# Kernel optimization log

Measured on AMD Instinct MI355X. Metric: run time of the kernel, lower is better.

## Reference

```python
import jax, jax.numpy as jnp
import numpy as np
import math

B, S, P, G = 8, 512, 64, 64
E, GE = 768, 32          # sub_embed_dim, gene_embed_dim
HD = E // 2              # sub_head_dim = 384
L = P * G
LAMBDA_INIT = 0.8 - 0.6 * math.exp(-0.3 * 0)  # depth=0 -> 0.2
SCALING = HD ** -0.5


def setup_inputs() -> dict:
    key0 = jax.random.key(0)
    ks = jax.random.split(key0, 12)
    init = 0.02
    return {
        "query": jax.random.normal(ks[0], (B, S, E), jnp.float32),
        "key": jax.random.normal(ks[1], (B, P, G, GE), jnp.float32),
        "query_mask": jax.random.bernoulli(ks[2], 0.9, (B, S)),
        "key_mask": jax.random.bernoulli(ks[3], 0.9, (B, P, G)),
        # weights stored [in, out] so y = x @ W (equiv to torch Linear no-bias)
        "Wq": jax.random.normal(ks[4], (E, E), jnp.float32) * init,
        "Wkv": jax.random.normal(ks[5], (GE, 2 * E), jnp.float32) * init,
        "Wout": jax.random.normal(ks[6], (E, E), jnp.float32) * init,
        "lambda_q1": jax.random.normal(ks[7], (HD,), jnp.float32) * 0.1,
        "lambda_k1": jax.random.normal(ks[8], (HD,), jnp.float32) * 0.1,
        "lambda_q2": jax.random.normal(ks[9], (HD,), jnp.float32) * 0.1,
        "lambda_k2": jax.random.normal(ks[10], (HD,), jnp.float32) * 0.1,
        "ln_weight": jnp.ones((E,), jnp.float32),  # RMSNorm affine weight (2*HD = E)
    }


def reference(query, key, query_mask, key_mask, Wq, Wkv, Wout,
              lambda_q1, lambda_k1, lambda_q2, lambda_k2, ln_weight):
    # Projections
    Q = query @ Wq                                   # [B,S,E]
    KV = key.reshape(B, L, GE) @ Wkv                 # [B,L,2E]
    K = KV[..., :E]                                  # [B,L,E]
    V = KV[..., E:]                                  # [B,L,E] (= 2*HD)

    # Split into 2 heads of dim HD
    Qh = Q.reshape(B, S, 2, HD).transpose(0, 2, 1, 3) * SCALING   # [B,2,S,HD]
    Kh = K.reshape(B, L, 2, HD).transpose(0, 2, 1, 3)             # [B,2,L,HD]

    # Combined mask [B,S,L]
    mask = query_mask[:, :, None] & key_mask.reshape(B, L)[:, None, :]

    # Dual attention scores + stable softmax (eps=1e-8 on denominator)
    scores = jnp.einsum('bhsd,bhld->bhsl', Qh, Kh)                # [B,2,S,L]
    scores = jnp.where(mask[:, None], scores, -1e20)
    m = jnp.max(scores, axis=-1, keepdims=True)
    p = jnp.exp(scores - m)
    attn = p / (jnp.sum(p, axis=-1, keepdims=True) + 1e-8)

    # Differential combination
    lam = (jnp.exp(jnp.sum(lambda_q1 * lambda_k1))
           - jnp.exp(jnp.sum(lambda_q2 * lambda_k2)) + LAMBDA_INIT)
    diff = attn[:, 0] - lam * attn[:, 1]                          # [B,S,L]
    diff = diff - jnp.min(diff, axis=-1, keepdims=True) + 1e-20
    diff = jnp.where(mask, diff, 0.0)

    # Value contraction: [B,S,L] @ [B,L,E] -> [B,S,E]
    attn_out = jnp.einsum('bsl,ble->bse', diff, V)

    # RMSNorm (eps=1e-5, affine) then scale by (1 - lambda_init)
    ms = jnp.mean(attn_out * attn_out, axis=-1, keepdims=True)
    attn_out = attn_out * jax.lax.rsqrt(ms + 1e-5) * ln_weight
    attn_out = attn_out * (1.0 - LAMBDA_INIT)

    out = attn_out @ Wout                                         # [B,S,E]
    return out, diff.reshape(B, S, P, G)
```

## Files before the change

### kernel.cpp

```cpp
#include <hip/hip_runtime.h>
#include <math.h>

#define LAM_INIT 0.2f
#define ONE_MINUS_LAM 0.8f
#define SCALING_F 0.05103103630798288f

typedef _Float16 h2 __attribute__((ext_vector_type(2)));

#if defined(__has_builtin)
#if __has_builtin(__builtin_amdgcn_fdot2)
#define FDOT2(a, b, c) __builtin_amdgcn_fdot2((a), (b), (c), false)
#endif
#endif
#ifndef FDOT2
#define FDOT2(a, b, c) ((float)(a).x * (float)(b).x + ((float)(a).y * (float)(b).y + (c)))
#endif

__device__ inline float waveMin(float v) {
#pragma unroll
    for (int o = 32; o > 0; o >>= 1) v = fminf(v, __shfl_xor(v, o));
    return v;
}
__device__ inline float waveSum(float v) {
#pragma unroll
    for (int o = 32; o > 0; o >>= 1) v += __shfl_xor(v, o);
    return v;
}

__global__ __launch_bounds__(256) void k01_prep(
    const float* __restrict__ key, const float* __restrict__ Wq,
    const float* __restrict__ Wkv, const float* __restrict__ Wout,
    const float* __restrict__ lq1, const float* __restrict__ lk1,
    const float* __restrict__ lq2, const float* __restrict__ lk2,
    const float* __restrict__ ln,
    unsigned* __restrict__ keyThU, float* __restrict__ Wcp,
    float* __restrict__ Wvp, float* __restrict__ lam)
{
    int blk = blockIdx.x;
    int tid = threadIdx.x;
    if (blk < 128) {
        int b  = blk >> 4;
        int l0 = (blk & 15) << 8;
        __shared__ float tile[256 * 33];
        const float* kp = key + ((size_t)b * 4096 + l0) * 32;
#pragma unroll
        for (int q = 0; q < 32; ++q) {
            int idx = tid + (q << 8);
            int r = idx >> 5, g = idx & 31;
            tile[r * 33 + g] = kp[idx];
        }
        __syncthreads();
#pragma unroll
        for (int gp = 0; gp < 16; ++gp) {
            h2 v;
            v.x = (_Float16)tile[tid * 33 + 2 * gp];
            v.y = (_Float16)tile[tid * 33 + 2 * gp + 1];
            keyThU[((size_t)(b * 16 + gp)) * 4096 + l0 + tid] =
                __builtin_bit_cast(unsigned, v);
        }
    } else if (blk < 512) {
        int bb = blk - 128;
        int kc = bb & 1;
        int ob = bb >> 1;
        int idx = ob * 256 + tid;
        int e  = idx >> 6;
        int hg = idx & 63;
        int h = hg >> 5, g = hg & 31;
        const float4* wqr = (const float4*)(Wq  + (size_t)e * 768 + h * 384 + kc * 192);
        const float4* wkr = (const float4*)(Wkv + (size_t)g * 1536 + h * 384 + kc * 192);
        float s0 = 0.f, s1 = 0.f;
#pragma unroll 4
        for (int d = 0; d < 48; d += 2) {
            float4 a0 = wqr[d],   b0 = wkr[d];
            float4 a1 = wqr[d+1], b1 = wkr[d+1];
            s0 += a0.x*b0.x + a0.y*b0.y + a0.z*b0.z + a0.w*b0.w;
            s1 += a1.x*b1.x + a1.y*b1.y + a1.z*b1.z + a1.w*b1.w;
        }
        Wcp[kc * 49152 + idx] = (s0 + s1) * SCALING_F;
    } else if (blk < 1280) {
        int bb = blk - 512;
        int kc = bb / 96;
        int ob = bb - kc * 96;
        int idx = ob * 256 + tid;
        int g = idx / 768;
        int e = idx - g * 768;
        const float* wvr = Wkv + (size_t)g * 1536 + 768;
        int c0 = kc * 96;
        float s0 = 0.f, s1 = 0.f;
#pragma unroll 4
        for (int c = c0; c < c0 + 96; c += 2) {
            s0 += wvr[c]   * ln[c]   * Wout[(size_t)c * 768 + e];
            s1 += wvr[c+1] * ln[c+1] * Wout[(size_t)(c+1) * 768 + e];
        }
        Wvp[kc * 24576 + idx] = s0 + s1;
    } else {
        float s1 = 0.f, s2 = 0.f;
        for (int d = tid; d < 384; d += 256) {
            s1 += lq1[d] * lk1[d];
            s2 += lq2[d] * lk2[d];
        }
        s1 = waveSum(s1);
        s2 = waveSum(s2);
        __shared__ float r1[4], r2[4];
        int wid = tid >> 6, lane = tid & 63;
        if (lane == 0) { r1[wid] = s1; r2[wid] = s2; }
        __syncthreads();
        if (tid == 0) {
            float a  = r1[0] + r1[1] + r1[2] + r1[3];
            float b2 = r2[0] + r2[1] + r2[2] + r2[3];
            lam[0] = expf(a) - expf(b2) + LAM_INIT;
        }
    }
}

__global__ __launch_bounds__(256) void k2_qt(
    const float* __restrict__ query, const float* __restrict__ Wcp,
    const float* __restrict__ Wvp, float* __restrict__ Wvo,
    float* __restrict__ Qtp)
{
    int blk = blockIdx.x;
    int tid = threadIdx.x;
    if (blk >= 512) {
        int idx = (blk - 512) * 256 + tid;
        float s = 0.f;
#pragma unroll
        for (int kc = 0; kc < 8; ++kc) s += Wvp[kc * 24576 + idx];
        Wvo[idx] = s;
        return;
    }
    int kc = blk >> 7;
    int mt = blk & 127;
    int m0 = mt * 32;
    __shared__ __align__(16) float As[64 * 33];
    __shared__ __align__(16) float Bs[64 * 64];

    int tm = tid >> 5;
    int tn = tid & 31;
    float acc[4][2];
#pragma unroll
    for (int r = 0; r < 4; ++r) { acc[r][0] = 0.f; acc[r][1] = 0.f; }

    for (int ch = 0; ch < 3; ++ch) {
        int k0 = kc * 192 + ch * 64;
        __syncthreads();
#pragma unroll
        for (int q = 0; q < 2; ++q) {
            int f = tid + q * 256;
            int m = f >> 4, kq = f & 15;
            float4 v = *(const float4*)&query[(size_t)(m0 + m) * 768 + k0 + kq * 4];
            As[(kq * 4 + 0) * 33 + m] = v.x;
            As[(kq * 4 + 1) * 33 + m] = v.y;
            As[(kq * 4 + 2) * 33 + m] = v.z;
            As[(kq * 4 + 3) * 33 + m] = v.w;
        }
#pragma unroll
        for (int q = 0; q < 4; ++q) {
            int f = tid + q * 256;
            int kk = f >> 4, n4 = f & 15;
            float4 a = *(const float4*)&Wcp[(size_t)(k0 + kk) * 64 + n4 * 4];
            float4 b = *(const float4*)&Wcp[49152 + (size_t)(k0 + kk) * 64 + n4 * 4];
            float4 s; s.x = a.x + b.x; s.y = a.y + b.y; s.z = a.z + b.z; s.w = a.w + b.w;
            *(float4*)&Bs[kk * 64 + n4 * 4] = s;
        }
        __syncthreads();
#pragma unroll 8
        for (int kk = 0; kk < 64; ++kk) {
            float4 a = *(const float4*)&As[kk * 33 + tm * 4];
            float2 b = *(const float2*)&Bs[kk * 64 + tn * 2];
            acc[0][0] += a.x * b.x; acc[0][1] += a.x * b.y;
            acc[1][0] += a.y * b.x; acc[1][1] += a.y * b.y;
            acc[2][0] += a.z * b.x; acc[2][1] += a.z * b.y;
            acc[3][0] += a.w * b.x; acc[3][1] += a.w * b.y;
        }
    }
#pragma unroll
    for (int r = 0; r < 4; ++r) {
        float2 o; o.x = acc[r][0]; o.y = acc[r][1];
        *(float2*)&Qtp[(size_t)kc * 262144 + (size_t)(m0 + tm * 4 + r) * 64 + tn * 2] = o;
    }
}

__global__ __launch_bounds__(512, 4) void k3_attn(
    const float* __restrict__ Qtp, const unsigned* __restrict__ keyThU,
    const int* __restrict__ qmask, const int* __restrict__ kmask,
    const float* __restrict__ lamp, float* __restrict__ diffO)
{
    int blk = blockIdx.x;
    int b  = blk >> 7;
    int s0 = (blk & 127) * 4;
    int tid = threadIdx.x;
    int lane = tid & 63, wid = tid >> 6;

    __shared__ __align__(16) unsigned qt_th[128];
    __shared__ float redS[64];
    __shared__ float redM[32];

    if (tid < 128) {
        int ts = tid >> 5;
        int h  = (tid >> 4) & 1;
        int gp = tid & 15;
        size_t row = (size_t)(b * 512 + s0 + ts) * 64;
        int col = h * 32 + 2 * gp;
        float v0 = 0.f, v1 = 0.f;
#pragma unroll
        for (int kc = 0; kc < 4; ++kc) {
            v0 += Qtp[(size_t)kc * 262144 + row + col];
            v1 += Qtp[(size_t)kc * 262144 + row + col + 1];
        }
        h2 hv; hv.x = (_Float16)v0; hv.y = (_Float16)v1;
        qt_th[gp * 8 + ts * 2 + h] = __builtin_bit_cast(unsigned, hv);
    }
    int qm[4];
#pragma unroll
    for (int ts = 0; ts < 4; ++ts) qm[ts] = qmask[b * 512 + s0 + ts];
    float lam = lamp[0];

    unsigned kmb = 0;
#pragma unroll
    for (int c = 0; c < 2; ++c) {
        int4 km = *(const int4*)(kmask + b * 4096 + c * 2048 + tid * 4);
        if (km.x) kmb |= 1u << (c * 4 + 0);
        if (km.y) kmb |= 1u << (c * 4 + 1);
        if (km.z) kmb |= 1u << (c * 4 + 2);
        if (km.w) kmb |= 1u << (c * 4 + 3);
    }
    __syncthreads();

    float p[2][4][8];
#pragma unroll
    for (int h = 0; h < 2; ++h)
#pragma unroll
        for (int ts = 0; ts < 4; ++ts)
#pragma unroll
            for (int i = 0; i < 8; ++i) p[h][ts][i] = 0.f;

    const unsigned* kt = keyThU + (size_t)b * 16 * 4096 + tid * 4;
    for (int gp = 0; gp < 16; ++gp) {
        uint4 q0 = *(const uint4*)&qt_th[gp * 8];
        uint4 q1 = *(const uint4*)&qt_th[gp * 8 + 4];
        h2 qv[8];
        qv[0] = __builtin_bit_cast(h2, q0.x); qv[1] = __builtin_bit_cast(h2, q0.y);
        qv[2] = __builtin_bit_cast(h2, q0.z); qv[3] = __builtin_bit_cast(h2, q0.w);
        qv[4] = __builtin_bit_cast(h2, q1.x); qv[5] = __builtin_bit_cast(h2, q1.y);
        qv[6] = __builtin_bit_cast(h2, q1.z); qv[7] = __builtin_bit_cast(h2, q1.w);
        const unsigned* kg = kt + (size_t)gp * 4096;
#pragma unroll
        for (int c = 0; c < 2; ++c) {
            uint4 kv = *(const uint4*)(kg + c * 2048);
            h2 k0 = __builtin_bit_cast(h2, kv.x);
            h2 k1 = __builtin_bit_cast(h2, kv.y);
            h2 k2 = __builtin_bit_cast(h2, kv.z);
            h2 k3 = __builtin_bit_cast(h2, kv.w);
#pragma unroll
            for (int ts = 0; ts < 4; ++ts)
#pragma unroll
                for (int h = 0; h < 2; ++h) {
                    h2 q = qv[ts * 2 + h];
                    p[h][ts][c*4+0] = FDOT2(k0, q, p[h][ts][c*4+0]);
                    p[h][ts][c*4+1] = FDOT2(k1, q, p[h][ts][c*4+1]);
                    p[h][ts][c*4+2] = FDOT2(k2, q, p[h][ts][c*4+2]);
                    p[h][ts][c*4+3] = FDOT2(k3, q, p[h][ts][c*4+3]);
                }
        }
    }

    float inv[2][4];
#pragma unroll
    for (int h = 0; h < 2; ++h)
#pragma unroll
        for (int ts = 0; ts < 4; ++ts) {
            float s = 0.f;
#pragma unroll
            for (int i = 0; i < 8; ++i) {
                bool ok = qm[ts] && ((kmb >> i) & 1u);
                float e = ok ? __expf(p[h][ts][i]) : 0.f;
                p[h][ts][i] = e;
                s += e;
            }
            s = waveSum(s);
            if (lane == 0) redS[(h * 4 + ts) * 8 + wid] = s;
        }
    __syncthreads();
#pragma unroll
    for (int h = 0; h < 2; ++h)
#pragma unroll
        for (int ts = 0; ts < 4; ++ts) {
            int r = (h * 4 + ts) * 8;
            float s = redS[r];
#pragma unroll
            for (int w = 1; w < 8; ++w) s += redS[r + w];
            inv[h][ts] = 1.0f / (s + 1e-8f);
        }

    float mn[4];
#pragma unroll
    for (int ts = 0; ts < 4; ++ts) {
        float v = 3.4e38f;
#pragma unroll
        for (int i = 0; i < 8; ++i) {
            float d = p[0][ts][i] * inv[0][ts] - lam * (p[1][ts][i] * inv[1][ts]);
            p[0][ts][i] = d;
            v = fminf(v, d);
        }
        v = waveMin(v);
        if (lane == 0) redM[ts * 8 + wid] = v;
    }
    __syncthreads();
#pragma unroll
    for (int ts = 0; ts < 4; ++ts) {
        int r = ts * 8;
        float v = redM[r];
#pragma unroll
        for (int w = 1; w < 8; ++w) v = fminf(v, redM[r + w]);
        mn[ts] = v;
    }

#pragma unroll
    for (int ts = 0; ts < 4; ++ts) {
        size_t base = (size_t)(b * 512 + s0 + ts) * 4096 + tid * 4;
#pragma unroll
        for (int c = 0; c < 2; ++c) {
            float4 o;
            float v0 = p[0][ts][c*4+0] - mn[ts] + 1e-20f;
            float v1 = p[0][ts][c*4+1] - mn[ts] + 1e-20f;
            float v2 = p[0][ts][c*4+2] - mn[ts] + 1e-20f;
            float v3 = p[0][ts][c*4+3] - mn[ts] + 1e-20f;
            o.x = (qm[ts] && ((kmb >> (c*4+0)) & 1u)) ? v0 : 0.f;
            o.y = (qm[ts] && ((kmb >> (c*4+1)) & 1u)) ? v1 : 0.f;
            o.z = (qm[ts] && ((kmb >> (c*4+2)) & 1u)) ? v2 : 0.f;
            o.w = (qm[ts] && ((kmb >> (c*4+3)) & 1u)) ? v3 : 0.f;
            *(float4*)(diffO + base + c * 2048) = o;
        }
    }
}

__global__ __launch_bounds__(256) void k4_T(
    const float* __restrict__ diff, const float* __restrict__ key,
    float* __restrict__ P)
{
    int blk = blockIdx.x;
    int rt = blk & 63, kc = blk >> 6;
    int row0 = rt << 6;
    int b = row0 >> 9;
    int l0 = kc << 9;
    int tid = threadIdx.x;
    int tx = tid & 7;
    int ty = tid >> 3;
    int g0 = tx * 4;

    __shared__ __align__(16) float Ks[256][32];

    float acc[2][4];
#pragma unroll
    for (int r = 0; r < 2; ++r)
#pragma unroll
        for (int c2 = 0; c2 < 4; ++c2) acc[r][c2] = 0.f;

    for (int ph = 0; ph < 2; ++ph) {
        int lp = l0 + ph * 256;
        __syncthreads();
#pragma unroll
        for (int q = 0; q < 32; ++q) {
            int idx = tid + (q << 8);
            int r = idx >> 5, g = idx & 31;
            Ks[r][g] = key[((size_t)(b * 4096 + lp + r)) * 32 + g];
        }
        __syncthreads();

        for (int j4 = 0; j4 < 64; ++j4) {
            int l = lp + j4 * 4;
            float4 dv[2];
#pragma unroll
            for (int r = 0; r < 2; ++r)
                dv[r] = *(const float4*)(diff + (size_t)(row0 + ty * 2 + r) * 4096 + l);
#pragma unroll
            for (int jj = 0; jj < 4; ++jj) {
                float4 kq = *(const float4*)&Ks[j4 * 4 + jj][g0];
#pragma unroll
                for (int r = 0; r < 2; ++r) {
                    float d = (jj == 0) ? dv[r].x : (jj == 1) ? dv[r].y : (jj == 2) ? dv[r].z : dv[r].w;
                    acc[r][0] += d * kq.x;
                    acc[r][1] += d * kq.y;
                    acc[r][2] += d * kq.z;
                    acc[r][3] += d * kq.w;
                }
            }
        }
    }
#pragma unroll
    for (int r = 0; r < 2; ++r) {
        float4 o; o.x = acc[r][0]; o.y = acc[r][1]; o.z = acc[r][2]; o.w = acc[r][3];
        *(float4*)&P[(size_t)kc * 131072 + (size_t)(row0 + ty * 2 + r) * 32 + g0] = o;
    }
}

__global__ __launch_bounds__(256, 4) void k5_out(
    const float* __restrict__ P, const float* __restrict__ Wkv,
    const float* __restrict__ Wvo, float* __restrict__ out)
{
    int row0 = blockIdx.x * 4;
    int tid = threadIdx.x;
    int w = tid >> 6;
    int lane = tid & 63;
    __shared__ __align__(16) float Ts[4][32];

    if (tid < 128) {
        int r = tid >> 5, g = tid & 31;
        float s = 0.f;
#pragma unroll
        for (int kc = 0; kc < 8; ++kc)
            s += P[(size_t)kc * 131072 + (size_t)(row0 + r) * 32 + g];
        Ts[r][g] = s;
    }
    __syncthreads();

    float4 t[8];
#pragma unroll
    for (int q = 0; q < 8; ++q) t[q] = *(const float4*)&Ts[w][q * 4];

    float ssq = 0.f;
#pragma unroll 2
    for (int j = 0; j < 12; ++j) {
        int e = lane + j * 64;
        const float* wp = Wkv + 768 + e;
        float a = 0.f;
#pragma unroll
        for (int q = 0; q < 8; ++q) {
            a += t[q].x * wp[(size_t)(q * 4 + 0) * 1536];
            a += t[q].y * wp[(size_t)(q * 4 + 1) * 1536];
            a += t[q].z * wp[(size_t)(q * 4 + 2) * 1536];
            a += t[q].w * wp[(size_t)(q * 4 + 3) * 1536];
        }
        ssq += a * a;
    }
    ssq = waveSum(ssq);
    float rs = rsqrtf(ssq * (1.0f / 768.0f) + 1e-5f) * ONE_MINUS_LAM;

#pragma unroll 2
    for (int j = 0; j < 12; ++j) {
        int e = lane + j * 64;
        const float* wp = Wvo + e;
        float o = 0.f;
#pragma unroll
        for (int q = 0; q < 8; ++q) {
            o += t[q].x * wp[(size_t)(q * 4 + 0) * 768];
            o += t[q].y * wp[(size_t)(q * 4 + 1) * 768];
            o += t[q].z * wp[(size_t)(q * 4 + 2) * 768];
            o += t[q].w * wp[(size_t)(q * 4 + 3) * 768];
        }
        out[(size_t)(row0 + w) * 768 + e] = o * rs;
    }
}

extern "C" void kernel_launch(void* const* d_in, const int* in_sizes, int n_in,
                              void* d_out, int out_size, void* d_ws, size_t ws_size,
                              hipStream_t stream) {
    (void)in_sizes; (void)n_in; (void)out_size; (void)ws_size;
    const float* query = (const float*)d_in[0];
    const float* key   = (const float*)d_in[1];
    const int*   qmask = (const int*)d_in[2];
    const int*   kmask = (const int*)d_in[3];
    const float* Wq    = (const float*)d_in[4];
    const float* Wkv   = (const float*)d_in[5];
    const float* Wout  = (const float*)d_in[6];
    const float* lq1   = (const float*)d_in[7];
    const float* lk1   = (const float*)d_in[8];
    const float* lq2   = (const float*)d_in[9];
    const float* lk2   = (const float*)d_in[10];
    const float* ln    = (const float*)d_in[11];

    float* out  = (float*)d_out;
    float* diff = out + 3145728;

    float* ws      = (float*)d_ws;
    float* Wcp     = ws;
    float* Wvo     = ws + 98304;
    float* Wvp     = ws + 122880;
    float* lam     = ws + 319488;
    unsigned* keyThU = (unsigned*)(ws + 319552);
    float* Qtp     = ws + 843840;
    float* P       = Qtp;

    k01_prep<<<1281, 256, 0, stream>>>(key, Wq, Wkv, Wout, lq1, lk1, lq2, lk2, ln,
                                       keyThU, Wcp, Wvp, lam);
    k2_qt<<<608, 256, 0, stream>>>(query, Wcp, Wvp, Wvo, Qtp);
    k3_attn<<<1024, 512, 0, stream>>>(Qtp, keyThU, qmask, kmask, lam, diff);
    k4_T<<<512, 256, 0, stream>>>(diff, key, P);
    k5_out<<<1024, 256, 0, stream>>>(P, Wkv, Wvo, out);
}
```

Baseline: 250.5 us.

## Compute RMSNorm sum of squares via precomputed Gram matrix and transpose Wvo

The RMSNorm sum of squares in the output kernel is rewritten as t^T M t, where M = Wv Wv^T is a 32x32 Gram matrix built in extra prep blocks. This replaces the 768-wide projection per row with 1024 small FMAs read from shared memory. Wvo is also stored transposed so each lane computes four output columns with float4 loads and writes a float4. The costs are four extra prep blocks and a strided transposed write in k2, plus a different floating-point summation order.

```diff
diff --git a/kernel.cpp b/kernel.cpp
--- a/kernel.cpp
+++ b/kernel.cpp
@@ -34,7 +34,8 @@
     const float* __restrict__ lq2, const float* __restrict__ lk2,
     const float* __restrict__ ln,
     unsigned* __restrict__ keyThU, float* __restrict__ Wcp,
-    float* __restrict__ Wvp, float* __restrict__ lam)
+    float* __restrict__ Wvp, float* __restrict__ lam,
+    float* __restrict__ M)
 {
     int blk = blockIdx.x;
     int tid = threadIdx.x;
@@ -93,7 +94,7 @@
             s1 += wvr[c+1] * ln[c+1] * Wout[(size_t)(c+1) * 768 + e];
         }
         Wvp[kc * 24576 + idx] = s0 + s1;
-    } else {
+    } else if (blk == 1280) {
         float s1 = 0.f, s2 = 0.f;
         for (int d = tid; d < 384; d += 256) {
             s1 += lq1[d] * lk1[d];
@@ -110,12 +111,24 @@
             float b2 = r2[0] + r2[1] + r2[2] + r2[3];
             lam[0] = expf(a) - expf(b2) + LAM_INIT;
         }
+    } else {
+        int idx = (blk - 1281) * 256 + tid;
+        int g = idx >> 5, gp = idx & 31;
+        const float4* ra = (const float4*)(Wkv + (size_t)g  * 1536 + 768);
+        const float4* rb = (const float4*)(Wkv + (size_t)gp * 1536 + 768);
+        float s = 0.f;
+#pragma unroll 4
+        for (int q = 0; q < 192; ++q) {
+            float4 a = ra[q], b = rb[q];
+            s += a.x*b.x + a.y*b.y + a.z*b.z + a.w*b.w;
+        }
+        M[idx] = s;
     }
 }
 
 __global__ __launch_bounds__(256) void k2_qt(
     const float* __restrict__ query, const float* __restrict__ Wcp,
-    const float* __restrict__ Wvp, float* __restrict__ Wvo,
+    const float* __restrict__ Wvp, float* __restrict__ WvoT,
     float* __restrict__ Qtp)
 {
     int blk = blockIdx.x;
@@ -125,7 +138,9 @@
         float s = 0.f;
 #pragma unroll
         for (int kc = 0; kc < 8; ++kc) s += Wvp[kc * 24576 + idx];
-        Wvo[idx] = s;
+        int g = idx / 768;
+        int e = idx - g * 768;
+        WvoT[(size_t)e * 32 + g] = s;
         return;
     }
     int kc = blk >> 7;
@@ -395,14 +410,15 @@
 }
 
 __global__ __launch_bounds__(256, 4) void k5_out(
-    const float* __restrict__ P, const float* __restrict__ Wkv,
-    const float* __restrict__ Wvo, float* __restrict__ out)
+    const float* __restrict__ P, const float* __restrict__ M,
+    const float* __restrict__ WvoT, float* __restrict__ out)
 {
     int row0 = blockIdx.x * 4;
     int tid = threadIdx.x;
     int w = tid >> 6;
     int lane = tid & 63;
     __shared__ __align__(16) float Ts[4][32];
+    __shared__ __align__(16) float Ml[1024];
 
     if (tid < 128) {
         int r = tid >> 5, g = tid & 31;
@@ -412,6 +428,8 @@
             s += P[(size_t)kc * 131072 + (size_t)(row0 + r) * 32 + g];
         Ts[r][g] = s;
     }
+#pragma unroll
+    for (int q = 0; q < 4; ++q) Ml[tid + q * 256] = M[tid + q * 256];
     __syncthreads();
 
     float4 t[8];
@@ -419,36 +437,33 @@
     for (int q = 0; q < 8; ++q) t[q] = *(const float4*)&Ts[w][q * 4];
 
     float ssq = 0.f;
-#pragma unroll 2
-    for (int j = 0; j < 12; ++j) {
-        int e = lane + j * 64;
-        const float* wp = Wkv + 768 + e;
-        float a = 0.f;
-#pragma unroll
-        for (int q = 0; q < 8; ++q) {
-            a += t[q].x * wp[(size_t)(q * 4 + 0) * 1536];
-            a += t[q].y * wp[(size_t)(q * 4 + 1) * 1536];
-            a += t[q].z * wp[(size_t)(q * 4 + 2) * 1536];
-            a += t[q].w * wp[(size_t)(q * 4 + 3) * 1536];
-        }
-        ssq += a * a;
+#pragma unroll
+    for (int i = 0; i < 16; ++i) {
+        int gg = lane + i * 64;
+        int g = gg >> 5, gp = gg & 31;
+        ssq = fmaf(Ts[w][g] * Ts[w][gp], Ml[gg], ssq);
     }
     ssq = waveSum(ssq);
     float rs = rsqrtf(ssq * (1.0f / 768.0f) + 1e-5f) * ONE_MINUS_LAM;
 
-#pragma unroll 2
-    for (int j = 0; j < 12; ++j) {
-        int e = lane + j * 64;
-        const float* wp = Wvo + e;
-        float o = 0.f;
+#pragma unroll
+    for (int j = 0; j < 3; ++j) {
+        int e0 = lane * 4 + j * 256;
+        const float4* wp = (const float4*)(WvoT + (size_t)e0 * 32);
+        float4 o; o.x = 0.f; o.y = 0.f; o.z = 0.f; o.w = 0.f;
 #pragma unroll
         for (int q = 0; q < 8; ++q) {
-            o += t[q].x * wp[(size_t)(q * 4 + 0) * 768];
-            o += t[q].y * wp[(size_t)(q * 4 + 1) * 768];
-            o += t[q].z * wp[(size_t)(q * 4 + 2) * 768];
-            o += t[q].w * wp[(size_t)(q * 4 + 3) * 768];
-        }
-        out[(size_t)(row0 + w) * 768 + e] = o * rs;
+            float4 a0 = wp[q];
+            float4 a1 = wp[q + 8];
+            float4 a2 = wp[q + 16];
+            float4 a3 = wp[q + 24];
+            o.x += t[q].x*a0.x + t[q].y*a0.y + t[q].z*a0.z + t[q].w*a0.w;
+            o.y += t[q].x*a1.x + t[q].y*a1.y + t[q].z*a1.z + t[q].w*a1.w;
+            o.z += t[q].x*a2.x + t[q].y*a2.y + t[q].z*a2.z + t[q].w*a2.w;
+            o.w += t[q].x*a3.x + t[q].y*a3.y + t[q].z*a3.z + t[q].w*a3.w;
+        }
+        o.x *= rs; o.y *= rs; o.z *= rs; o.w *= rs;
+        *(float4*)(out + (size_t)(row0 + w) * 768 + e0) = o;
     }
 }
 
@@ -474,17 +489,18 @@
 
     float* ws      = (float*)d_ws;
     float* Wcp     = ws;
-    float* Wvo     = ws + 98304;
+    float* WvoT    = ws + 98304;
     float* Wvp     = ws + 122880;
     float* lam     = ws + 319488;
     unsigned* keyThU = (unsigned*)(ws + 319552);
     float* Qtp     = ws + 843840;
     float* P       = Qtp;
-
-    k01_prep<<<1281, 256, 0, stream>>>(key, Wq, Wkv, Wout, lq1, lk1, lq2, lk2, ln,
-                                       keyThU, Wcp, Wvp, lam);
-    k2_qt<<<608, 256, 0, stream>>>(query, Wcp, Wvp, Wvo, Qtp);
+    float* Mbuf    = ws + 1892416;
+
+    k01_prep<<<1285, 256, 0, stream>>>(key, Wq, Wkv, Wout, lq1, lk1, lq2, lk2, ln,
+                                       keyThU, Wcp, Wvp, lam, Mbuf);
+    k2_qt<<<608, 256, 0, stream>>>(query, Wcp, Wvp, WvoT, Qtp);
     k3_attn<<<1024, 512, 0, stream>>>(Qtp, keyThU, qmask, kmask, lam, diff);
     k4_T<<<512, 256, 0, stream>>>(diff, key, P);
-    k5_out<<<1024, 256, 0, stream>>>(P, Wkv, Wvo, out);
-}
+    k5_out<<<1024, 256, 0, stream>>>(P, Mbuf, WvoT, out);
+}
```

Measured after the change: 275.9 us. +10.2%, slower.
